# Optimization experiments

Hardware: AMD Instinct MI355X
Metric: run time of the kernel (lower is better)

The kernel has to match this reference:

```python
import jax, jax.numpy as jnp
import numpy as np

N_HEADS = 32
D_MODEL = 1024
D_K = D_MODEL // N_HEADS  # 32; must equal N_HEADS for the module's broadcast to be valid
B, S = 2, 2048


def setup_inputs() -> dict:
    key = jax.random.key(0)
    ks = jax.random.split(key, 6)
    s = 0.02
    return {
        "x": jax.random.normal(ks[0], (B, S, D_MODEL), jnp.float32),
        "Wq": jax.random.normal(ks[1], (D_MODEL, D_MODEL), jnp.float32) * s,
        "bq": jnp.zeros((D_MODEL,), jnp.float32),
        "Wk": jax.random.normal(ks[2], (D_MODEL, D_K), jnp.float32) * s,
        "bk": jnp.zeros((D_K,), jnp.float32),
        "Wv": jax.random.normal(ks[3], (D_MODEL, D_K), jnp.float32) * s,
        "bv": jnp.zeros((D_K,), jnp.float32),
        "Wo": jax.random.normal(ks[4], (D_MODEL, D_MODEL), jnp.float32) * s,
        "bo": jnp.zeros((D_MODEL,), jnp.float32),
    }


def reference(x, Wq, bq, Wk, bk, Wv, bv, Wo, bo):
    b, s_len, d = x.shape
    q = x @ Wq + bq                 # (B,S,D)
    k = x @ Wk + bk                 # (B,S,D_K) -- single shared K head (MQA)
    v = x @ Wv + bv                 # (B,S,D_K)
    # Faithful to torch: view(B,S,d_k,n_heads).transpose(1,2) -> (B, D_K, S, N_HEADS)
    # The 'a' axis (size D_K) acts as the broadcast batch axis paired with the
    # expanded K/V head axis (size N_HEADS); valid because D_K == N_HEADS.
    q = q.reshape(b, s_len, D_K, N_HEADS).transpose(0, 2, 1, 3)  # (B,A,S,H)
    scores = jnp.einsum('bash,bth->bast', q, k) / jnp.sqrt(jnp.float32(D_K))  # (B,A,S,S)
    w = jax.nn.softmax(scores, axis=-1)
    out = jnp.einsum('bast,bte->base', w, v)  # (B,A,S,D_K)
    out = out.transpose(0, 2, 1, 3).reshape(b, s_len, d)  # (B,S,D)
    return out @ Wo + bo
```

## Files before the change

kernel.cpp:

```cpp
#include <hip/hip_runtime.h>
#include <cstdint>
#include <cstddef>

typedef unsigned short u16;
typedef unsigned int u32;
typedef __attribute__((ext_vector_type(8))) short short8;
typedef __attribute__((ext_vector_type(4))) float f32x4;

#define S_LEN 2048
#define NBATCH 2
#define DM 1024
#define DK 32
#define NH 32
#define M_ROWS 4096
#define SCALE 0.17677669529663687f

__device__ __forceinline__ u16 bf16_rne(float f) {
  u32 u = __float_as_uint(f);
  u32 r = (u + 0x7FFFu + ((u >> 16) & 1u)) >> 16;
  return (u16)r;
}
__device__ __forceinline__ void split2(float x, u16& hi, u16& lo) {
  u32 u = __float_as_uint(x);
  hi = (u16)(u >> 16);
  float hif = __uint_as_float(u & 0xFFFF0000u);
  lo = bf16_rne(x - hif);
}
__device__ __forceinline__ u32 pack2(float lo, float hi) {
  return (u32)bf16_rne(lo) | ((u32)bf16_rne(hi) << 16);
}
__device__ __forceinline__ void gl16(const u16* gsrc, u16* ldst) {
  __builtin_amdgcn_global_load_lds((const u32*)gsrc, (u32*)ldst, 16, 0, 0);
}

__global__ __launch_bounds__(256)
void split_x(const float* __restrict__ X, u16* __restrict__ Hi,
             u16* __restrict__ Lo) {
  const size_t i0 = ((size_t)blockIdx.x * 256 + threadIdx.x) * 8;
  const float4 v0 = *(const float4*)(X + i0);
  const float4 v1 = *(const float4*)(X + i0 + 4);
  const float f[8] = {v0.x, v0.y, v0.z, v0.w, v1.x, v1.y, v1.z, v1.w};
  u16 h[8], l[8];
#pragma unroll
  for (int e = 0; e < 8; ++e) split2(f[e], h[e], l[e]);
  uint4 hv, lv;
  hv.x = h[0] | ((u32)h[1] << 16); hv.y = h[2] | ((u32)h[3] << 16);
  hv.z = h[4] | ((u32)h[5] << 16); hv.w = h[6] | ((u32)h[7] << 16);
  lv.x = l[0] | ((u32)l[1] << 16); lv.y = l[2] | ((u32)l[3] << 16);
  lv.z = l[4] | ((u32)l[5] << 16); lv.w = l[6] | ((u32)l[7] << 16);
  *(uint4*)(Hi + i0) = hv;
  *(uint4*)(Lo + i0) = lv;
}

__global__ __launch_bounds__(256)
void tsplit(const float* __restrict__ W, u16* __restrict__ Thi,
            u16* __restrict__ Tlo) {
  __shared__ float tile[32][33];
  const int k0 = blockIdx.x * 32, n0 = blockIdx.y * 32;
  const int tx = threadIdx.x & 31, ty = threadIdx.x >> 5;
#pragma unroll
  for (int i = 0; i < 4; ++i)
    tile[ty + 8 * i][tx] = W[(size_t)(k0 + ty + 8 * i) * DM + n0 + tx];
  __syncthreads();
#pragma unroll
  for (int i = 0; i < 4; ++i) {
    const float v = tile[tx][ty + 8 * i];
    u16 h, l;
    split2(v, h, l);
    const size_t d = (size_t)(n0 + ty + 8 * i) * DM + k0 + tx;
    Thi[d] = h;
    Tlo[d] = l;
  }
}

template <int QMODE>
__global__ __launch_bounds__(256, 2)
void gemm2(const u16* __restrict__ Ahi, const u16* __restrict__ Alo,
           const u16* __restrict__ Bhi, const u16* __restrict__ Blo,
           const float* __restrict__ bias, float* __restrict__ C,
           u16* __restrict__ Ohi, u16* __restrict__ Olo) {
  __shared__ u16 ldsA[2][2][8][64][8];
  __shared__ u16 ldsB[2][2][4][64][8];
  const int t = threadIdx.x;
  const int wvi = t >> 6, l = t & 63;
  const int bid = blockIdx.x;
  const int wg = ((bid & 7) << 6) | (bid >> 3);
  const int m0 = (wg >> 4) * 128;
  const int n0 = (wg & 15) * 64;
  const int wr = wvi >> 1, wc = wvi & 1;
  const int lrow = l & 15, lk = (l >> 4) * 8;

  const u16* sbase =
      (wvi == 0) ? Ahi : (wvi == 1) ? Alo : (wvi == 2) ? Bhi : Blo;
  const int srow0 = (wvi < 2) ? m0 : n0;

  f32x4 acc[4][2];
#pragma unroll
  for (int i = 0; i < 4; ++i)
#pragma unroll
    for (int j = 0; j < 2; ++j) acc[i][j] = (f32x4){0.f, 0.f, 0.f, 0.f};

  auto issue = [&](int buf, int kk) {
    if (wvi < 2) {
#pragma unroll
      for (int mt = 0; mt < 8; ++mt)
        gl16(sbase + (size_t)(srow0 + mt * 16 + lrow) * DM + kk + lk,
             &ldsA[buf][wvi][mt][0][0]);
    } else {
#pragma unroll
      for (int nt = 0; nt < 4; ++nt)
        gl16(sbase + (size_t)(srow0 + nt * 16 + lrow) * DM + kk + lk,
             &ldsB[buf][wvi - 2][nt][0][0]);
    }
  };

  issue(0, 0);
  for (int ks = 0; ks < 32; ++ks) {
    const int cb = ks & 1;
    __syncthreads();
    if (ks < 31) issue(cb ^ 1, (ks + 1) * 32);

    short8 ah[4], alo[4], bh[2], bl[2];
#pragma unroll
    for (int i = 0; i < 4; ++i) {
      ah[i] = *(const short8*)&ldsA[cb][0][wr * 4 + i][l][0];
      alo[i] = *(const short8*)&ldsA[cb][1][wr * 4 + i][l][0];
    }
#pragma unroll
    for (int j = 0; j < 2; ++j) {
      bh[j] = *(const short8*)&ldsB[cb][0][wc * 2 + j][l][0];
      bl[j] = *(const short8*)&ldsB[cb][1][wc * 2 + j][l][0];
    }
#pragma unroll
    for (int i = 0; i < 4; ++i)
#pragma unroll
      for (int j = 0; j < 2; ++j) {
        acc[i][j] = __builtin_amdgcn_mfma_f32_16x16x32_bf16(ah[i], bh[j],
                                                            acc[i][j], 0, 0, 0);
        acc[i][j] = __builtin_amdgcn_mfma_f32_16x16x32_bf16(ah[i], bl[j],
                                                            acc[i][j], 0, 0, 0);
        acc[i][j] = __builtin_amdgcn_mfma_f32_16x16x32_bf16(alo[i], bh[j],
                                                            acc[i][j], 0, 0, 0);
      }
  }

  const int lcol = l & 15;
  float bj[2];
#pragma unroll
  for (int j = 0; j < 2; ++j) bj[j] = bias[n0 + wc * 32 + j * 16 + lcol];
#pragma unroll
  for (int i = 0; i < 4; ++i) {
    const int row0 = m0 + wr * 64 + i * 16 + (l >> 4) * 4;
#pragma unroll
    for (int j = 0; j < 2; ++j) {
      const int coln = n0 + wc * 32 + j * 16 + lcol;
#pragma unroll
      for (int q = 0; q < 4; ++q) {
        const float val = acc[i][j][q] + bj[j];
        if constexpr (QMODE == 0) {
          C[(size_t)(row0 + q) * DM + coln] = val;
        } else {
          u16 hh, ll;
          split2(val * SCALE, hh, ll);
          Ohi[(size_t)(row0 + q) * DM + coln] = hh;
          Olo[(size_t)(row0 + q) * DM + coln] = ll;
        }
      }
    }
  }
}

__global__ __launch_bounds__(256)
void kv_proj(const float* __restrict__ X, const float* __restrict__ Wk,
             const float* __restrict__ bk, const float* __restrict__ Wv,
             const float* __restrict__ bv, u16* __restrict__ Khi,
             u16* __restrict__ Klo, u16* __restrict__ Vthi,
             u16* __restrict__ Vtlo) {
  const int col = threadIdx.x & 63;
  const int rr = threadIdx.x >> 6;
  const int row = blockIdx.x * 4 + rr;
  const float* __restrict__ xr = X + (size_t)row * DM;
  const bool isK = col < DK;
  const int cc = isK ? col : col - DK;
  const float* __restrict__ w = (isK ? Wk : Wv) + cc;
  float acc = isK ? bk[cc] : bv[cc];
#pragma unroll 8
  for (int k = 0; k < DM; ++k) acc = fmaf(xr[k], w[(size_t)k * DK], acc);
  u16 h, l;
  split2(acc, h, l);
  if (isK) {
    Khi[(size_t)row * DK + cc] = h;
    Klo[(size_t)row * DK + cc] = l;
  } else {
    const size_t d =
        (size_t)(row >> 11) * DK * S_LEN + (size_t)cc * S_LEN + (row & 2047);
    Vthi[d] = h;
    Vtlo[d] = l;
  }
}

__global__ __launch_bounds__(256, 4)
void flash_mfma2(const u16* __restrict__ Qhi, const u16* __restrict__ Qlo,
                 const u16* __restrict__ Khi, const u16* __restrict__ Klo,
                 const u16* __restrict__ Vthi, const u16* __restrict__ Vtlo,
                 u16* __restrict__ Ohi, u16* __restrict__ Olo) {
  __shared__ u16 stg[2][4][2][64][8];
  __shared__ u16 plds[4][2][64][8];
  const int a = blockIdx.y, b = blockIdx.z;
  const int tid = threadIdx.x;
  const int wv = tid >> 6, l = tid & 63;
  const int lq = l & 15, lc = l >> 4;
  const int q0w = blockIdx.x * 128 + wv * 32;
  const size_t bS = (size_t)b * S_LEN;
  const size_t bDS = (size_t)b * DK * S_LEN;

  short8 qh[2], ql[2];
#pragma unroll
  for (int mt = 0; mt < 2; ++mt) {
    const size_t off =
        (size_t)(b * S_LEN + q0w + mt * 16 + lq) * DM + a * DK + lc * 8;
    qh[mt] = *(const short8*)(Qhi + off);
    ql[mt] = *(const short8*)(Qlo + off);
  }

  f32x4 oacc[2][2];
#pragma unroll
  for (int mt = 0; mt < 2; ++mt)
#pragma unroll
    for (int et = 0; et < 2; ++et) oacc[mt][et] = (f32x4){0.f, 0.f, 0.f, 0.f};
  float lsum[2] = {0.f, 0.f};

  const u16* kbase = (wv == 0) ? Khi : Klo;
  const u16* vbase = (wv == 2) ? Vthi : Vtlo;

  auto issue = [&](int buf, int t0) {
    if (wv < 2) {
#pragma unroll
      for (int tt = 0; tt < 2; ++tt)
        gl16(kbase + (bS + t0 + tt * 16 + lq) * DK + lc * 8,
             &stg[buf][wv][tt][0][0]);
    } else {
#pragma unroll
      for (int tt = 0; tt < 2; ++tt)
        gl16(vbase + bDS + (size_t)(tt * 16 + lq) * S_LEN + t0 + lc * 8,
             &stg[buf][wv][tt][0][0]);
    }
  };

  issue(0, 0);
  for (int it = 0; it < 64; ++it) {
    const int cb = it & 1;
    __syncthreads();
    if (it < 63) issue(cb ^ 1, (it + 1) * 32);

    short8 kh[2], klo[2], vh[2], vl[2];
#pragma unroll
    for (int tt = 0; tt < 2; ++tt) {
      kh[tt] = *(const short8*)&stg[cb][0][tt][l][0];
      klo[tt] = *(const short8*)&stg[cb][1][tt][l][0];
      vh[tt] = *(const short8*)&stg[cb][2][tt][l][0];
      vl[tt] = *(const short8*)&stg[cb][3][tt][l][0];
    }
#pragma unroll
    for (int mt = 0; mt < 2; ++mt) {
      f32x4 s0 = (f32x4){0.f, 0.f, 0.f, 0.f};
      f32x4 s1 = (f32x4){0.f, 0.f, 0.f, 0.f};
      s0 = __builtin_amdgcn_mfma_f32_16x16x32_bf16(kh[0], qh[mt], s0, 0, 0, 0);
      s0 = __builtin_amdgcn_mfma_f32_16x16x32_bf16(kh[0], ql[mt], s0, 0, 0, 0);
      s0 = __builtin_amdgcn_mfma_f32_16x16x32_bf16(klo[0], qh[mt], s0, 0, 0, 0);
      s1 = __builtin_amdgcn_mfma_f32_16x16x32_bf16(kh[1], qh[mt], s1, 0, 0, 0);
      s1 = __builtin_amdgcn_mfma_f32_16x16x32_bf16(kh[1], ql[mt], s1, 0, 0, 0);
      s1 = __builtin_amdgcn_mfma_f32_16x16x32_bf16(klo[1], qh[mt], s1, 0, 0, 0);
      const float e0 = __expf(s0[0]), e1 = __expf(s0[1]);
      const float e2 = __expf(s0[2]), e3 = __expf(s0[3]);
      const float e4 = __expf(s1[0]), e5 = __expf(s1[1]);
      const float e6 = __expf(s1[2]), e7 = __expf(s1[3]);
      lsum[mt] += ((e0 + e1) + (e2 + e3)) + ((e4 + e5) + (e6 + e7));
      const u32 pA = pack2(e0, e1), pB = pack2(e2, e3);
      const u32 pC = pack2(e4, e5), pD = pack2(e6, e7);
      const int fl1 = ((lc >> 1) << 4) | lq;
      const int fl2 = (((lc >> 1) + 2) << 4) | lq;
      *(uint2*)&plds[wv][mt][fl1][(lc & 1) * 4] = make_uint2(pA, pB);
      *(uint2*)&plds[wv][mt][fl2][(lc & 1) * 4] = make_uint2(pC, pD);
    }
#pragma unroll
    for (int mt = 0; mt < 2; ++mt) {
      const short8 pf = *(const short8*)&plds[wv][mt][l][0];
      oacc[mt][0] = __builtin_amdgcn_mfma_f32_16x16x32_bf16(pf, vh[0],
                                                            oacc[mt][0], 0, 0, 0);
      oacc[mt][0] = __builtin_amdgcn_mfma_f32_16x16x32_bf16(pf, vl[0],
                                                            oacc[mt][0], 0, 0, 0);
      oacc[mt][1] = __builtin_amdgcn_mfma_f32_16x16x32_bf16(pf, vh[1],
                                                            oacc[mt][1], 0, 0, 0);
      oacc[mt][1] = __builtin_amdgcn_mfma_f32_16x16x32_bf16(pf, vl[1],
                                                            oacc[mt][1], 0, 0, 0);
    }
  }

#pragma unroll
  for (int mt = 0; mt < 2; ++mt) {
    float s = lsum[mt];
    s += __shfl_xor(s, 16);
    s += __shfl_xor(s, 32);
    const float inv = 1.f / s;
    float invr[4];
#pragma unroll
    for (int rg = 0; rg < 4; ++rg)
      invr[rg] = __int_as_float(__builtin_amdgcn_ds_bpermute(
          (((lc << 2) | rg)) << 2, __float_as_int(inv)));
    const size_t rb = (size_t)(b * S_LEN + q0w + mt * 16 + lc * 4);
#pragma unroll
    for (int et = 0; et < 2; ++et) {
#pragma unroll
      for (int rg = 0; rg < 4; ++rg) {
        const float val = oacc[mt][et][rg] * invr[rg];
        u16 hh, ll;
        split2(val, hh, ll);
        const size_t idx = (rb + rg) * DM + a * DK + et * 16 + lq;
        Ohi[idx] = hh;
        Olo[idx] = ll;
      }
    }
  }
}

extern "C" void kernel_launch(void* const* d_in, const int* in_sizes, int n_in,
                              void* d_out, int out_size, void* d_ws,
                              size_t ws_size, hipStream_t stream) {
  const float* x  = (const float*)d_in[0];
  const float* Wq = (const float*)d_in[1];
  const float* bq = (const float*)d_in[2];
  const float* Wk = (const float*)d_in[3];
  const float* bk = (const float*)d_in[4];
  const float* Wv = (const float*)d_in[5];
  const float* bv = (const float*)d_in[6];
  const float* Wo = (const float*)d_in[7];
  const float* bo = (const float*)d_in[8];
  float* out = (float*)d_out;

  char* ws = (char*)d_ws;
  const size_t MB = 1024 * 1024;
  u16* Xhi = (u16*)ws;
  u16* Xlo = (u16*)(ws + 8 * MB);
  u16* Khi  = (u16*)(ws + 16 * MB);
  u16* Klo  = (u16*)(ws + 16 * MB + 256 * 1024);
  u16* Vthi = (u16*)(ws + 16 * MB + 512 * 1024);
  u16* Vtlo = (u16*)(ws + 16 * MB + 768 * 1024);
  u16* Wqthi = (u16*)(ws + 17 * MB);
  u16* Wqtlo = (u16*)(ws + 19 * MB);
  u16* Wothi = (u16*)(ws + 21 * MB);
  u16* Wotlo = (u16*)(ws + 23 * MB);
  u16* Qhi = (u16*)d_out;
  u16* Qlo = Qhi + (size_t)M_ROWS * DM;

  hipLaunchKernelGGL(split_x, dim3(2048), dim3(256), 0, stream, x, Xhi, Xlo);
  hipLaunchKernelGGL(tsplit, dim3(32, 32), dim3(256), 0, stream, Wq, Wqthi,
                     Wqtlo);
  hipLaunchKernelGGL(tsplit, dim3(32, 32), dim3(256), 0, stream, Wo, Wothi,
                     Wotlo);
  hipLaunchKernelGGL(kv_proj, dim3(M_ROWS / 4), dim3(256), 0, stream, x, Wk,
                     bk, Wv, bv, Khi, Klo, Vthi, Vtlo);
  hipLaunchKernelGGL(HIP_KERNEL_NAME(gemm2<1>), dim3(512), dim3(256), 0,
                     stream, Xhi, Xlo, Wqthi, Wqtlo, bq, (float*)nullptr, Qhi,
                     Qlo);
  hipLaunchKernelGGL(flash_mfma2, dim3(16, NH, NBATCH), dim3(256), 0, stream,
                     Qhi, Qlo, Khi, Klo, Vthi, Vtlo, Xhi, Xlo);
  hipLaunchKernelGGL(HIP_KERNEL_NAME(gemm2<0>), dim3(512), dim3(256), 0,
                     stream, Xhi, Xlo, Wothi, Wotlo, bo, out, (u16*)nullptr,
                     (u16*)nullptr);
}
```

Baseline: 348.9 us.

## Triple-buffer LDS staging in GEMM and flash kernels with explicit vmcnt waits

Moves the GEMM and flash-attention kernels from double to triple LDS buffering. They prefetch two tiles ahead and replace __syncthreads with a partial s_waitcnt vmcnt plus a raw s_barrier, so global-to-LDS loads overlap more compute. It also rewrites pack2 to use the HIP bf16 conversion intrinsics. The extra buffer raises LDS use per block, which may limit occupancy. Correctness also depends on the hand-counted vmcnt values matching the number of outstanding loads per wave.

```diff
diff --git a/kernel.cpp b/kernel.cpp
--- a/kernel.cpp
+++ b/kernel.cpp
@@ -1,4 +1,5 @@
 #include <hip/hip_runtime.h>
+#include <hip/hip_bf16.h>
 #include <cstdint>
 #include <cstddef>
 
@@ -26,8 +27,11 @@
   float hif = __uint_as_float(u & 0xFFFF0000u);
   lo = bf16_rne(x - hif);
 }
-__device__ __forceinline__ u32 pack2(float lo, float hi) {
-  return (u32)bf16_rne(lo) | ((u32)bf16_rne(hi) << 16);
+__device__ __forceinline__ u32 pack2(float a, float b) {
+  __hip_bfloat162 v;
+  v.x = __float2bfloat16(a);
+  v.y = __float2bfloat16(b);
+  return *(u32*)&v;
 }
 __device__ __forceinline__ void gl16(const u16* gsrc, u16* ldst) {
   __builtin_amdgcn_global_load_lds((const u32*)gsrc, (u32*)ldst, 16, 0, 0);
@@ -75,12 +79,12 @@
 
 template <int QMODE>
 __global__ __launch_bounds__(256, 2)
-void gemm2(const u16* __restrict__ Ahi, const u16* __restrict__ Alo,
+void gemm3(const u16* __restrict__ Ahi, const u16* __restrict__ Alo,
            const u16* __restrict__ Bhi, const u16* __restrict__ Blo,
            const float* __restrict__ bias, float* __restrict__ C,
            u16* __restrict__ Ohi, u16* __restrict__ Olo) {
-  __shared__ u16 ldsA[2][2][8][64][8];
-  __shared__ u16 ldsB[2][2][4][64][8];
+  __shared__ u16 ldsA[3][2][8][64][8];
+  __shared__ u16 ldsB[3][2][4][64][8];
   const int t = threadIdx.x;
   const int wvi = t >> 6, l = t & 63;
   const int bid = blockIdx.x;
@@ -115,10 +119,19 @@
   };
 
   issue(0, 0);
+  issue(1, 32);
   for (int ks = 0; ks < 32; ++ks) {
-    const int cb = ks & 1;
-    __syncthreads();
-    if (ks < 31) issue(cb ^ 1, (ks + 1) * 32);
+    if (ks == 31) {
+      asm volatile("s_waitcnt vmcnt(0)" ::: "memory");
+    } else if (wvi < 2) {
+      asm volatile("s_waitcnt vmcnt(8)" ::: "memory");
+    } else {
+      asm volatile("s_waitcnt vmcnt(4)" ::: "memory");
+    }
+    __builtin_amdgcn_s_barrier();
+    __builtin_amdgcn_sched_barrier(0);
+    if (ks < 30) issue((ks + 2) % 3, (ks + 2) * 32);
+    const int cb = ks % 3;
 
     short8 ah[4], alo[4], bh[2], bl[2];
 #pragma unroll
@@ -200,11 +213,11 @@
 }
 
 __global__ __launch_bounds__(256, 4)
-void flash_mfma2(const u16* __restrict__ Qhi, const u16* __restrict__ Qlo,
-                 const u16* __restrict__ Khi, const u16* __restrict__ Klo,
-                 const u16* __restrict__ Vthi, const u16* __restrict__ Vtlo,
-                 u16* __restrict__ Ohi, u16* __restrict__ Olo) {
-  __shared__ u16 stg[2][4][2][64][8];
+void flash3(const u16* __restrict__ Qhi, const u16* __restrict__ Qlo,
+            const u16* __restrict__ Khi, const u16* __restrict__ Klo,
+            const u16* __restrict__ Vthi, const u16* __restrict__ Vtlo,
+            u16* __restrict__ Ohi, u16* __restrict__ Olo) {
+  __shared__ u16 stg[3][4][2][64][8];
   __shared__ u16 plds[4][2][64][8];
   const int a = blockIdx.y, b = blockIdx.z;
   const int tid = threadIdx.x;
@@ -248,10 +261,17 @@
   };
 
   issue(0, 0);
+  issue(1, 32);
   for (int it = 0; it < 64; ++it) {
-    const int cb = it & 1;
-    __syncthreads();
-    if (it < 63) issue(cb ^ 1, (it + 1) * 32);
+    if (it == 63) {
+      asm volatile("s_waitcnt vmcnt(0)" ::: "memory");
+    } else {
+      asm volatile("s_waitcnt vmcnt(2)" ::: "memory");
+    }
+    __builtin_amdgcn_s_barrier();
+    __builtin_amdgcn_sched_barrier(0);
+    if (it < 62) issue((it + 2) % 3, (it + 2) * 32);
+    const int cb = it % 3;
 
     short8 kh[2], klo[2], vh[2], vl[2];
 #pragma unroll
@@ -360,12 +380,12 @@
                      Wotlo);
   hipLaunchKernelGGL(kv_proj, dim3(M_ROWS / 4), dim3(256), 0, stream, x, Wk,
                      bk, Wv, bv, Khi, Klo, Vthi, Vtlo);
-  hipLaunchKernelGGL(HIP_KERNEL_NAME(gemm2<1>), dim3(512), dim3(256), 0,
+  hipLaunchKernelGGL(HIP_KERNEL_NAME(gemm3<1>), dim3(512), dim3(256), 0,
                      stream, Xhi, Xlo, Wqthi, Wqtlo, bq, (float*)nullptr, Qhi,
                      Qlo);
-  hipLaunchKernelGGL(flash_mfma2, dim3(16, NH, NBATCH), dim3(256), 0, stream,
+  hipLaunchKernelGGL(flash3, dim3(16, NH, NBATCH), dim3(256), 0, stream,
                      Qhi, Qlo, Khi, Klo, Vthi, Vtlo, Xhi, Xlo);
-  hipLaunchKernelGGL(HIP_KERNEL_NAME(gemm2<0>), dim3(512), dim3(256), 0,
+  hipLaunchKernelGGL(HIP_KERNEL_NAME(gemm3<0>), dim3(512), dim3(256), 0,
                      stream, Xhi, Xlo, Wothi, Wotlo, bo, out, (u16*)nullptr,
                      (u16*)nullptr);
 }
```

Measured after the change: 342.6 us. About the same (-1.8%).
